# Kernel tuning notes

Measured on AMD Instinct MI355X. Metric: run time of the kernel, lower is better.

Reference implementation:

```python
import jax, jax.numpy as jnp
import numpy as np

ROPE_BASE = 10000.0

def _rope_tables(seq_len, head_dim, dtype):
    inv_freq = 1.0 / (ROPE_BASE ** (jnp.arange(0, head_dim, 2, dtype=jnp.float32) / head_dim))
    t = jnp.arange(seq_len, dtype=jnp.float32)
    freqs = jnp.einsum('s,d->sd', t, inv_freq)  # [S, D/2]
    return jnp.cos(freqs).astype(dtype), jnp.sin(freqs).astype(dtype)

def _apply_rope(x, cos, sin):
    # x: [B, H, S, D]; cos/sin: [S, D/2]
    half = x.shape[-1] // 2
    x1, x2 = x[..., :half], x[..., half:]
    c = cos[None, None, :, :]
    s = sin[None, None, :, :]
    return jnp.concatenate([x1 * c - x2 * s, x1 * s + x2 * c], axis=-1)

def setup_inputs() -> dict:
    key = jax.random.key(0)
    k1, k2, k3 = jax.random.split(key, 3)
    B, S, dim = 4, 2048, 1024
    x = jax.random.normal(k1, (B, S, dim), dtype=jnp.float32)
    Wqkv = jax.random.normal(k2, (3 * dim, dim), dtype=jnp.float32) * (1.0 / np.sqrt(dim))
    Wout = jax.random.normal(k3, (dim, dim), dtype=jnp.float32) * (1.0 / np.sqrt(dim))
    mask = jnp.tril(jnp.ones((S, S), dtype=bool))[None, None, :, :]  # causal [1,1,S,S]
    return {"x": x, "mask": mask, "Wqkv": Wqkv, "Wout": Wout, "n_heads": 16}

def reference(x, mask, Wqkv, Wout, n_heads):
    B, S, dim = x.shape
    H = n_heads
    D = dim // H
    qkv = jnp.einsum('bsd,ed->bse', x, Wqkv)             # [B,S,3*dim]
    qkv = qkv.reshape(B, S, 3, H, D)
    q = jnp.transpose(qkv[:, :, 0], (0, 2, 1, 3))        # [B,H,S,D]
    k = jnp.transpose(qkv[:, :, 1], (0, 2, 1, 3))
    v = jnp.transpose(qkv[:, :, 2], (0, 2, 1, 3))
    cos, sin = _rope_tables(S, D, x.dtype)
    q = _apply_rope(q, cos, sin)
    k = _apply_rope(k, cos, sin)
    scale = 1.0 / np.sqrt(D).astype(np.float32)
    scores = jnp.einsum('bhsd,bhtd->bhst', q, k) * scale  # [B,H,S,S]
    scores = jnp.where(mask, scores, -jnp.inf)
    attn = jax.nn.softmax(scores, axis=-1)
    out = jnp.einsum('bhst,bhtd->bhsd', attn, v)          # [B,H,S,D]
    out = jnp.transpose(out, (0, 2, 1, 3)).reshape(B, S, dim)
    return jnp.einsum('bsd,ed->bse', out, Wout)
```

## Files before the change

kernel.cpp:

```cpp
#include <hip/hip_runtime.h>
#include <math.h>


typedef __attribute__((ext_vector_type(8))) __bf16 bf16x8;
typedef __attribute__((ext_vector_type(8))) short  short8;
typedef __attribute__((ext_vector_type(4))) short  s16x4;
typedef __attribute__((ext_vector_type(4))) float  f32x4;

#define MFMA16(a, b, c) __builtin_amdgcn_mfma_f32_16x16x32_bf16((a), (b), (c), 0, 0, 0)

static constexpr int    BATCH = 4;
static constexpr int    SEQ   = 2048;
static constexpr int    DIM   = 1024;
static constexpr int    NH    = 16;
static constexpr int    HD    = 64;
static constexpr size_t BHSD  = (size_t)BATCH * NH * SEQ * HD;
static constexpr float  NEGINF = -1e9f;
static constexpr int    PS_LD  = 72;

__device__ __forceinline__ short f2bf(float f) {
    union { float f; unsigned u; } v; v.f = f;
    unsigned r = v.u + 0x7fffu + ((v.u >> 16) & 1u);
    return (short)(r >> 16);
}

__device__ __forceinline__ short8 cvt8(const f32x4 lo, const f32x4 hi) {
    short8 r;
    r[0] = f2bf(lo[0]); r[1] = f2bf(lo[1]); r[2] = f2bf(lo[2]); r[3] = f2bf(lo[3]);
    r[4] = f2bf(hi[0]); r[5] = f2bf(hi[1]); r[6] = f2bf(hi[2]); r[7] = f2bf(hi[3]);
    return r;
}

template <bool F32>
__device__ __forceinline__ short8 ld8(const void* p, size_t row, int K, int k) {
    if constexpr (F32) {
        const float* f = (const float*)p;
        f32x4 lo = *(const f32x4*)&f[row * (size_t)K + k];
        f32x4 hi = *(const f32x4*)&f[row * (size_t)K + k + 4];
        return cvt8(lo, hi);
    } else {
        const short* s = (const short*)p;
        return *(const short8*)&s[row * (size_t)K + k];
    }
}

template <bool AF32, bool BF32>
__device__ __forceinline__ void gemm128_core(
    const void* __restrict__ A, const void* __restrict__ B, int K,
    short* As, short* Bs, int bm, int bn, f32x4 acc[4][4]) {
    const int tid  = threadIdx.x;
    const int lane = tid & 63;
    const int wave = tid >> 6;
    const int quad = lane >> 4;
    const int col  = lane & 15;
    const int wm   = (wave & 1) * 64;
    const int wn   = (wave >> 1) * 64;

    const int r0 = tid >> 2;
    const int r1 = (tid + 256) >> 2;
    const int ko = (tid & 3) * 8;

#pragma unroll
    for (int i = 0; i < 4; ++i)
#pragma unroll
        for (int j = 0; j < 4; ++j) acc[i][j] = f32x4{0.f, 0.f, 0.f, 0.f};

#pragma unroll 1
    for (int k0 = 0; k0 < K; k0 += 32) {
        short8 a0 = ld8<AF32>(A, (size_t)(bm + r0), K, k0 + ko);
        short8 a1 = ld8<AF32>(A, (size_t)(bm + r1), K, k0 + ko);
        short8 b0 = ld8<BF32>(B, (size_t)(bn + r0), K, k0 + ko);
        short8 b1 = ld8<BF32>(B, (size_t)(bn + r1), K, k0 + ko);
        __syncthreads();
        *(short8*)&As[tid * 8]         = a0;
        *(short8*)&As[(tid + 256) * 8] = a1;
        *(short8*)&Bs[tid * 8]         = b0;
        *(short8*)&Bs[(tid + 256) * 8] = b1;
        __syncthreads();

        bf16x8 af[4], bfr[4];
#pragma unroll
        for (int i = 0; i < 4; ++i)
            af[i] = *(const bf16x8*)&As[(wm + i * 16 + col) * 32 + quad * 8];
#pragma unroll
        for (int j = 0; j < 4; ++j)
            bfr[j] = *(const bf16x8*)&Bs[(wn + j * 16 + col) * 32 + quad * 8];
#pragma unroll
        for (int i = 0; i < 4; ++i)
#pragma unroll
            for (int j = 0; j < 4; ++j)
                acc[i][j] = MFMA16(af[i], bfr[j], acc[i][j]);
    }
}

__global__ __launch_bounds__(256, 2) void qkv_rope_kernel(
    const float* __restrict__ X, const float* __restrict__ W,
    short* __restrict__ Qo, short* __restrict__ Ko, short* __restrict__ VT) {
    __shared__ __align__(16) short As[128 * 32];
    __shared__ __align__(16) short Bs[128 * 32];
    const int bm = blockIdx.y * 128, bn = blockIdx.x * 128;
    const int lane = threadIdx.x & 63, wave = threadIdx.x >> 6;
    const int quad = lane >> 4, col = lane & 15;
    const int wm = (wave & 1) * 64, wn = (wave >> 1) * 64;

    f32x4 acc[4][4];
    gemm128_core<true, true>(X, W, 1024, As, Bs, bm, bn, acc);

    const int n0    = bn + wn;
    const int which = n0 >> 10;
    const int h     = (n0 >> 6) & 15;

    if (which == 2) {
#pragma unroll
        for (int i = 0; i < 4; ++i) {
            int    m = bm + wm + i * 16 + quad * 4;
            int    b = m >> 11, s = m & 2047;
            size_t rowb = (size_t)(b * NH + h) * HD;
#pragma unroll
            for (int j = 0; j < 4; ++j) {
                int   d = j * 16 + col;
                s16x4 pk;
                pk[0] = f2bf(acc[i][j][0]); pk[1] = f2bf(acc[i][j][1]);
                pk[2] = f2bf(acc[i][j][2]); pk[3] = f2bf(acc[i][j][3]);
                *(s16x4*)&VT[(rowb + d) * SEQ + s] = pk;
            }
        }
    } else {
        short* dst = which ? Ko : Qo;
#pragma unroll
        for (int i = 0; i < 4; ++i)
#pragma unroll
            for (int reg = 0; reg < 4; ++reg) {
                int    m = bm + wm + i * 16 + quad * 4 + reg;
                int    b = m >> 11, s = m & 2047;
                size_t base = ((size_t)(b * NH + h) * SEQ + s) * HD;
#pragma unroll
                for (int j = 0; j < 2; ++j) {
                    int   d1  = j * 16 + col;
                    float inv = __expf(-0.28782313662425574f * (float)d1);
                    float ang = (float)s * inv;
                    float sn, cs;
                    sincosf(ang, &sn, &cs);
                    float x1 = acc[i][j][reg];
                    float x2 = acc[i][j + 2][reg];
                    dst[base + d1]      = f2bf(x1 * cs - x2 * sn);
                    dst[base + d1 + 32] = f2bf(x1 * sn + x2 * cs);
                }
            }
    }
}

__global__ __launch_bounds__(256, 2) void attn_kernel(
    const short* __restrict__ Q, const short* __restrict__ K,
    const short* __restrict__ VT, short* __restrict__ att) {
    const int b = blockIdx.z, h = blockIdx.y;
    const int tid = threadIdx.x, wave = tid >> 6, lane = tid & 63;
    const int quad = lane >> 4, col = lane & 15;
    const size_t hoff = (size_t)(b * NH + h) * SEQ * HD;
    const short* Qp  = Q + hoff;
    const short* Kp  = K + hoff;
    const short* VTp = VT + hoff;

    __shared__ __align__(16) short Kt[64 * 64];
    __shared__ __align__(16) short Vt[64 * 64];
    __shared__ __align__(16) short Ps[4 * 16 * PS_LD];

    const int r0 = tid >> 3;
    const int r1 = r0 + 32;
    const int c8 = (tid & 7) * 8;
    const int cs = c8 ^ ((r0 & 7) << 3);
    const int swc = (col & 7) << 3;
    const int cA  = (quad * 8) ^ swc;
    const int cB  = (32 + quad * 8) ^ swc;
    short* Pw = &Ps[wave * 16 * PS_LD];

#pragma unroll 1
    for (int pass = 0; pass < 2; ++pass) {
        const int qt = pass ? 31 - (int)blockIdx.x : (int)blockIdx.x;
        const int q0 = qt * 64 + wave * 16;

        bf16x8 aq0 = *(const bf16x8*)&Qp[(q0 + col) * HD + quad * 8];
        bf16x8 aq1 = *(const bf16x8*)&Qp[(q0 + col) * HD + 32 + quad * 8];

        float m_i[4], l_i[4];
        f32x4 o[4];
#pragma unroll
        for (int r = 0; r < 4; ++r) { m_i[r] = NEGINF; l_i[r] = 0.f; o[r] = f32x4{0.f, 0.f, 0.f, 0.f}; }

        short8 ka = *(const short8*)&Kp[r0 * HD + c8];
        short8 kb = *(const short8*)&Kp[r1 * HD + c8];
        short8 va = *(const short8*)&VTp[(size_t)r0 * SEQ + c8];
        short8 vb = *(const short8*)&VTp[(size_t)r1 * SEQ + c8];

#pragma unroll 1
        for (int t = 0; t <= qt; ++t) {
            const int kt = t * 64;
            __syncthreads();
            *(short8*)&Kt[r0 * 64 + cs] = ka;
            *(short8*)&Kt[r1 * 64 + cs] = kb;
            *(short8*)&Vt[r0 * 64 + cs] = va;
            *(short8*)&Vt[r1 * 64 + cs] = vb;
            __syncthreads();

            if (t < qt) {
                const int kn = kt + 64;
                ka = *(const short8*)&Kp[(kn + r0) * HD + c8];
                kb = *(const short8*)&Kp[(kn + r1) * HD + c8];
                va = *(const short8*)&VTp[(size_t)r0 * SEQ + kn + c8];
                vb = *(const short8*)&VTp[(size_t)r1 * SEQ + kn + c8];
            }

            float p[4][4];
#pragma unroll
            for (int jn = 0; jn < 4; ++jn) {
                f32x4  s  = f32x4{0.f, 0.f, 0.f, 0.f};
                bf16x8 b0 = *(const bf16x8*)&Kt[(jn * 16 + col) * 64 + cA];
                bf16x8 b1 = *(const bf16x8*)&Kt[(jn * 16 + col) * 64 + cB];
                s = MFMA16(aq0, b0, s);
                s = MFMA16(aq1, b1, s);
                if (t == qt) {
#pragma unroll
                    for (int reg = 0; reg < 4; ++reg) {
                        int qr = wave * 16 + quad * 4 + reg;
                        int kc = jn * 16 + col;
                        p[jn][reg] = (kc <= qr) ? s[reg] * 0.125f : NEGINF;
                    }
                } else {
#pragma unroll
                    for (int reg = 0; reg < 4; ++reg) p[jn][reg] = s[reg] * 0.125f;
                }
            }

            float alpha[4];
#pragma unroll
            for (int reg = 0; reg < 4; ++reg) {
                float mx = fmaxf(fmaxf(p[0][reg], p[1][reg]), fmaxf(p[2][reg], p[3][reg]));
#pragma unroll
                for (int off = 8; off >= 1; off >>= 1) mx = fmaxf(mx, __shfl_xor(mx, off, 64));
                float mn   = fmaxf(m_i[reg], mx);
                alpha[reg] = __expf(m_i[reg] - mn);
                float rs = 0.f;
#pragma unroll
                for (int jn = 0; jn < 4; ++jn) { p[jn][reg] = __expf(p[jn][reg] - mn); rs += p[jn][reg]; }
#pragma unroll
                for (int off = 8; off >= 1; off >>= 1) rs += __shfl_xor(rs, off, 64);
                l_i[reg] = l_i[reg] * alpha[reg] + rs;
                m_i[reg] = mn;
            }
#pragma unroll
            for (int jd = 0; jd < 4; ++jd)
#pragma unroll
                for (int reg = 0; reg < 4; ++reg) o[jd][reg] *= alpha[reg];

#pragma unroll
            for (int jn = 0; jn < 4; ++jn)
#pragma unroll
                for (int reg = 0; reg < 4; ++reg)
                    Pw[(quad * 4 + reg) * PS_LD + jn * 16 + col] = f2bf(p[jn][reg]);

            bf16x8 ap0 = *(const bf16x8*)&Pw[col * PS_LD + quad * 8];
            bf16x8 ap1 = *(const bf16x8*)&Pw[col * PS_LD + 32 + quad * 8];
#pragma unroll
            for (int jd = 0; jd < 4; ++jd) {
                bf16x8 bv0 = *(const bf16x8*)&Vt[(jd * 16 + col) * 64 + cA];
                bf16x8 bv1 = *(const bf16x8*)&Vt[(jd * 16 + col) * 64 + cB];
                o[jd] = MFMA16(ap0, bv0, o[jd]);
                o[jd] = MFMA16(ap1, bv1, o[jd]);
            }
        }

#pragma unroll
        for (int jd = 0; jd < 4; ++jd)
#pragma unroll
            for (int reg = 0; reg < 4; ++reg) {
                int s = q0 + quad * 4 + reg;
                att[((size_t)(b * SEQ + s)) * DIM + h * HD + jd * 16 + col] =
                    f2bf(o[jd][reg] / l_i[reg]);
            }
    }
}

__global__ __launch_bounds__(256, 2) void out_gemm_kernel(
    const short* __restrict__ A, const float* __restrict__ W,
    float* __restrict__ out) {
    __shared__ __align__(16) short As[128 * 32];
    __shared__ __align__(16) short Bs[128 * 32];
    const int bm = blockIdx.y * 128, bn = blockIdx.x * 128;
    const int lane = threadIdx.x & 63, wave = threadIdx.x >> 6;
    const int quad = lane >> 4, col = lane & 15;
    const int wm = (wave & 1) * 64, wn = (wave >> 1) * 64;

    f32x4 acc[4][4];
    gemm128_core<false, true>(A, W, 1024, As, Bs, bm, bn, acc);

#pragma unroll
    for (int i = 0; i < 4; ++i)
#pragma unroll
        for (int reg = 0; reg < 4; ++reg) {
            int    m    = bm + wm + i * 16 + quad * 4 + reg;
            size_t base = (size_t)m * DIM + bn + wn;
#pragma unroll
            for (int j = 0; j < 4; ++j)
                out[base + j * 16 + col] = acc[i][j][reg];
        }
}

extern "C" void kernel_launch(void* const* d_in, const int* in_sizes, int n_in,
                              void* d_out, int out_size, void* d_ws, size_t ws_size,
                              hipStream_t stream) {
    const float* x    = nullptr;
    const float* Wqkv = nullptr;
    const float* Wout = nullptr;
    for (int i = 0; i < n_in; ++i) {
        switch (in_sizes[i]) {
            case 8388608: x    = (const float*)d_in[i]; break;
            case 3145728: Wqkv = (const float*)d_in[i]; break;
            case 1048576: Wout = (const float*)d_in[i]; break;
            default: break;
        }
    }
    if (!x || !Wqkv || !Wout) return;

    short* Q  = (short*)d_ws;
    short* K  = Q + BHSD;
    short* VT = K + BHSD;
    float* out = (float*)d_out;

    qkv_rope_kernel<<<dim3(24, 64), 256, 0, stream>>>(x, Wqkv, Q, K, VT);

    const bool direct = ws_size >= (size_t)4 * BHSD * sizeof(short);
    short* att_dst = direct ? (VT + BHSD) : (short*)d_out;
    attn_kernel<<<dim3(16, NH, BATCH), 256, 0, stream>>>(Q, K, VT, att_dst);

    short* att = att_dst;
    if (!direct) {
        att = (short*)d_ws;
        hipMemcpyAsync(att, att_dst, BHSD * sizeof(short), hipMemcpyDeviceToDevice, stream);
    }
    out_gemm_kernel<<<dim3(8, 64), 256, 0, stream>>>(att, Wout, out);
}
```

Baseline: 346.7 us.

## Precast inputs and weights to bf16 and precompute RoPE tables in prep kernel

Adds a prep kernel that converts X, Wqkv and Wout from fp32 to bf16 once and fills cos/sin RoPE tables in workspace. The QKV and output GEMMs then load bf16 directly instead of converting fp32 tiles on every load, and the RoPE epilogue reads table values instead of calling exp and sincos. This adds an extra kernel launch and an extra pass over inputs and weights, and it needs more workspace, with the old path kept as a fallback.

```diff
diff --git a/kernel.cpp b/kernel.cpp
--- a/kernel.cpp
+++ b/kernel.cpp
@@ -41,6 +41,33 @@
     } else {
         const short* s = (const short*)p;
         return *(const short8*)&s[row * (size_t)K + k];
+    }
+}
+
+__global__ __launch_bounds__(256) void prep_kernel(
+    const float* __restrict__ X, const float* __restrict__ Wq,
+    const float* __restrict__ Wo, short* __restrict__ Xb,
+    short* __restrict__ Wqb, short* __restrict__ Wob,
+    float* __restrict__ cosT, float* __restrict__ sinT) {
+    const int stride = gridDim.x * blockDim.x;
+    for (int idx = blockIdx.x * blockDim.x + threadIdx.x; idx < 3211264; idx += stride) {
+        if (idx < 3145728) {
+            const float* src; short* dst; int off;
+            if (idx < 2097152)      { src = X;  dst = Xb;  off = idx; }
+            else if (idx < 2883584) { src = Wq; dst = Wqb; off = idx - 2097152; }
+            else                    { src = Wo; dst = Wob; off = idx - 2883584; }
+            f32x4 v = *(const f32x4*)&src[(size_t)off * 4];
+            s16x4 r;
+            r[0] = f2bf(v[0]); r[1] = f2bf(v[1]); r[2] = f2bf(v[2]); r[3] = f2bf(v[3]);
+            *(s16x4*)&dst[(size_t)off * 4] = r;
+        } else {
+            int r = idx - 3145728;
+            int s = r >> 5, d = r & 31;
+            float ang = (float)s * __expf(-0.28782313662425574f * (float)d);
+            float sn, cs;
+            sincosf(ang, &sn, &cs);
+            cosT[r] = cs; sinT[r] = sn;
+        }
     }
 }
 
@@ -93,8 +120,10 @@
     }
 }
 
+template <bool PRE>
 __global__ __launch_bounds__(256, 2) void qkv_rope_kernel(
-    const float* __restrict__ X, const float* __restrict__ W,
+    const void* __restrict__ X, const void* __restrict__ W,
+    const float* __restrict__ cosT, const float* __restrict__ sinT,
     short* __restrict__ Qo, short* __restrict__ Ko, short* __restrict__ VT) {
     __shared__ __align__(16) short As[128 * 32];
     __shared__ __align__(16) short Bs[128 * 32];
@@ -104,7 +133,7 @@
     const int wm = (wave & 1) * 64, wn = (wave >> 1) * 64;
 
     f32x4 acc[4][4];
-    gemm128_core<true, true>(X, W, 1024, As, Bs, bm, bn, acc);
+    gemm128_core<!PRE, !PRE>(X, W, 1024, As, Bs, bm, bn, acc);
 
     const int n0    = bn + wn;
     const int which = n0 >> 10;
@@ -136,11 +165,15 @@
                 size_t base = ((size_t)(b * NH + h) * SEQ + s) * HD;
 #pragma unroll
                 for (int j = 0; j < 2; ++j) {
-                    int   d1  = j * 16 + col;
-                    float inv = __expf(-0.28782313662425574f * (float)d1);
-                    float ang = (float)s * inv;
+                    int   d1 = j * 16 + col;
                     float sn, cs;
-                    sincosf(ang, &sn, &cs);
+                    if constexpr (PRE) {
+                        cs = cosT[(s << 5) + d1];
+                        sn = sinT[(s << 5) + d1];
+                    } else {
+                        float inv = __expf(-0.28782313662425574f * (float)d1);
+                        sincosf((float)s * inv, &sn, &cs);
+                    }
                     float x1 = acc[i][j][reg];
                     float x2 = acc[i][j + 2][reg];
                     dst[base + d1]      = f2bf(x1 * cs - x2 * sn);
@@ -280,8 +313,9 @@
     }
 }
 
+template <bool PRE>
 __global__ __launch_bounds__(256, 2) void out_gemm_kernel(
-    const short* __restrict__ A, const float* __restrict__ W,
+    const short* __restrict__ A, const void* __restrict__ W,
     float* __restrict__ out) {
     __shared__ __align__(16) short As[128 * 32];
     __shared__ __align__(16) short Bs[128 * 32];
@@ -291,7 +325,7 @@
     const int wm = (wave & 1) * 64, wn = (wave >> 1) * 64;
 
     f32x4 acc[4][4];
-    gemm128_core<false, true>(A, W, 1024, As, Bs, bm, bn, acc);
+    gemm128_core<false, !PRE>(A, W, 1024, As, Bs, bm, bn, acc);
 
 #pragma unroll
     for (int i = 0; i < 4; ++i)
@@ -326,16 +360,37 @@
     short* VT = K + BHSD;
     float* out = (float*)d_out;
 
-    qkv_rope_kernel<<<dim3(24, 64), 256, 0, stream>>>(x, Wqkv, Q, K, VT);
-
-    const bool direct = ws_size >= (size_t)4 * BHSD * sizeof(short);
-    short* att_dst = direct ? (VT + BHSD) : (short*)d_out;
-    attn_kernel<<<dim3(16, NH, BATCH), 256, 0, stream>>>(Q, K, VT, att_dst);
-
-    short* att = att_dst;
-    if (!direct) {
-        att = (short*)d_ws;
-        hipMemcpyAsync(att, att_dst, BHSD * sizeof(short), hipMemcpyDeviceToDevice, stream);
-    }
-    out_gemm_kernel<<<dim3(8, 64), 256, 0, stream>>>(att, Wout, out);
-}
+    const size_t need_pre = (size_t)4 * BHSD * sizeof(short)
+                          + BHSD * sizeof(short)
+                          + (size_t)3145728 * sizeof(short)
+                          + (size_t)1048576 * sizeof(short)
+                          + (size_t)2 * 65536 * sizeof(float);
+
+    if (ws_size >= need_pre) {
+        short* att  = VT + BHSD;
+        short* Xb   = att + BHSD;
+        short* Wqb  = Xb + BHSD;
+        short* Wob  = Wqb + 3145728;
+        float* cosT = (float*)(Wob + 1048576);
+        float* sinT = cosT + 65536;
+
+        prep_kernel<<<dim3(2048), 256, 0, stream>>>(x, Wqkv, Wout, Xb, Wqb, Wob, cosT, sinT);
+        qkv_rope_kernel<true><<<dim3(24, 64), 256, 0, stream>>>(Xb, Wqb, cosT, sinT, Q, K, VT);
+        attn_kernel<<<dim3(16, NH, BATCH), 256, 0, stream>>>(Q, K, VT, att);
+        out_gemm_kernel<true><<<dim3(8, 64), 256, 0, stream>>>(att, Wob, out);
+    } else {
+        qkv_rope_kernel<false><<<dim3(24, 64), 256, 0, stream>>>(
+            x, Wqkv, nullptr, nullptr, Q, K, VT);
+
+        const bool direct = ws_size >= (size_t)4 * BHSD * sizeof(short);
+        short* att_dst = direct ? (VT + BHSD) : (short*)d_out;
+        attn_kernel<<<dim3(16, NH, BATCH), 256, 0, stream>>>(Q, K, VT, att_dst);
+
+        short* att = att_dst;
+        if (!direct) {
+            att = (short*)d_ws;
+            hipMemcpyAsync(att, att_dst, BHSD * sizeof(short), hipMemcpyDeviceToDevice, stream);
+        }
+        out_gemm_kernel<false><<<dim3(8, 64), 256, 0, stream>>>(att, Wout, out);
+    }
+}
```

New measurement: 315.9 us. 8.9% less time.
